# Performance work log

Measured on AMD Instinct MI355X. Metric: run time of the kernel, lower is better.

The kernel has to match this reference:

```python
import jax, jax.numpy as jnp
import numpy as np

CHANNELS = 512
GROUPS = 32
EPS = 1e-6


def setup_inputs() -> dict:
    key = jax.random.key(0)
    ks = jax.random.split(key, 10)
    C = CHANNELS
    s = 1.0 / np.sqrt(C)
    return {
        "hidden_states": jax.random.normal(ks[0], (4, 64, 64, C), dtype=jnp.float32),
        "gn_scale": jnp.ones((C,), dtype=jnp.float32),
        "gn_bias": jnp.zeros((C,), dtype=jnp.float32),
        "wq": jax.random.normal(ks[1], (C, C), dtype=jnp.float32) * s,
        "bq": jnp.zeros((C,), dtype=jnp.float32),
        "wk": jax.random.normal(ks[2], (C, C), dtype=jnp.float32) * s,
        "bk": jnp.zeros((C,), dtype=jnp.float32),
        "wv": jax.random.normal(ks[3], (C, C), dtype=jnp.float32) * s,
        "bv": jnp.zeros((C,), dtype=jnp.float32),
        "wo": jax.random.normal(ks[4], (C, C), dtype=jnp.float32) * s,
        "bo": jnp.zeros((C,), dtype=jnp.float32),
    }


def reference(hidden_states, gn_scale, gn_bias, wq, bq, wk, bk, wv, bv, wo, bo):
    B, H, W, C = hidden_states.shape
    residual = hidden_states
    L = H * W
    x = hidden_states.reshape(B, L, C)

    # GroupNorm: stats over (spatial, channels-within-group), per batch per group
    xg = x.reshape(B, L, GROUPS, C // GROUPS)
    mean = jnp.mean(xg, axis=(1, 3), keepdims=True)
    var = jnp.var(xg, axis=(1, 3), keepdims=True)
    xn = ((xg - mean) * jax.lax.rsqrt(var + EPS)).reshape(B, L, C)
    xn = xn * gn_scale + gn_bias

    # QKV projections (heads=1, head_dim=C)
    q = xn @ wq + bq
    k = xn @ wk + bk
    v = xn @ wv + bv

    scale = 1.0 / jnp.sqrt(jnp.asarray(C, dtype=q.dtype))
    scores = jnp.einsum('bld,bsd->bls', q, k) * scale  # [B, L, L]
    attn = jax.nn.softmax(scores, axis=-1)
    out = jnp.einsum('bls,bsd->bld', attn, v)

    out = out @ wo + bo
    return out.reshape(B, H, W, C) + residual
```

## Files before the change

kernel.cpp:

```cpp
#include <hip/hip_runtime.h>
#include <hip/hip_bf16.h>
#include <stdint.h>

#define BATCH 4
#define SEQ   4096
#define CH    512
#define NGRP  32
#define GEPS  1e-6f

typedef short  short8  __attribute__((ext_vector_type(8)));
typedef float  floatx4 __attribute__((ext_vector_type(4)));

static __device__ __forceinline__ short bf16b(float f) {
    __hip_bfloat16 h = __float2bfloat16(f);
    return __builtin_bit_cast(short, h);
}
static __device__ __forceinline__ float bf2f(short s) {
    unsigned u = ((unsigned)(unsigned short)s) << 16;
    return __builtin_bit_cast(float, u);
}
static __device__ __forceinline__ char fp8b(float f) {
    int pk = __builtin_amdgcn_cvt_pk_fp8_f32(f, f, 0, false);
    return (char)(pk & 0xff);
}

static __device__ __forceinline__ void dma16(const void* g, void* l) {
    __builtin_amdgcn_global_load_lds(
        (const __attribute__((address_space(1))) unsigned int*)g,
        (__attribute__((address_space(3))) unsigned int*)l, 16, 0, 0);
}

static __device__ __forceinline__ float rowmax16(float x) {
    int xi = __builtin_bit_cast(int, x);
    x = fmaxf(x, __builtin_bit_cast(float, __builtin_amdgcn_update_dpp(xi, xi, 0x128, 0xf, 0xf, true)));
    xi = __builtin_bit_cast(int, x);
    x = fmaxf(x, __builtin_bit_cast(float, __builtin_amdgcn_update_dpp(xi, xi, 0x124, 0xf, 0xf, true)));
    xi = __builtin_bit_cast(int, x);
    x = fmaxf(x, __builtin_bit_cast(float, __builtin_amdgcn_update_dpp(xi, xi, 0x122, 0xf, 0xf, true)));
    xi = __builtin_bit_cast(int, x);
    x = fmaxf(x, __builtin_bit_cast(float, __builtin_amdgcn_update_dpp(xi, xi, 0x121, 0xf, 0xf, true)));
    return x;
}

__global__ __launch_bounds__(256) void gn_partial_kernel(const float* __restrict__ x,
                                                         float* __restrict__ statsraw) {
    int blk = blockIdx.x;
    int t = threadIdx.x;
    size_t row0 = (size_t)blk * 64;
    int qd = t & 127;
    int rh = t >> 7;
    const float* base = x + row0 * 512 + qd * 4;
    float s1 = 0.f, s2 = 0.f;
    #pragma unroll 4
    for (int i = 0; i < 32; ++i) {
        int r = rh + i * 2;
        float4 v = *reinterpret_cast<const float4*>(base + (size_t)r * 512);
        s1 += v.x + v.y + v.z + v.w;
        s2 += v.x * v.x + v.y * v.y + v.z * v.z + v.w * v.w;
    }
    __shared__ float a1[256], a2[256];
    a1[t] = s1; a2[t] = s2;
    __syncthreads();
    if (t < 32) {
        float u1 = 0.f, u2 = 0.f;
        #pragma unroll
        for (int e = 0; e < 4; ++e) {
            u1 += a1[t * 4 + e] + a1[128 + t * 4 + e];
            u2 += a2[t * 4 + e] + a2[128 + t * 4 + e];
        }
        int b = (int)(row0 >> 12);
        atomicAdd(&statsraw[(b * 32 + t) * 2],     u1);
        atomicAdd(&statsraw[(b * 32 + t) * 2 + 1], u2);
    }
}

__global__ __launch_bounds__(256) void gn_apply_kernel(const float* __restrict__ x,
                                                       const float* __restrict__ statsraw,
                                                       const float* __restrict__ gsc,
                                                       const float* __restrict__ gbs,
                                                       short* __restrict__ xn) {
    int i4 = blockIdx.x * 256 + threadIdx.x;
    int base = i4 * 4;
    int b = base >> 21;
    int c = base & 511;
    int sidx = (b * 32 + (c >> 4)) * 2;
    float s1 = statsraw[sidx], s2 = statsraw[sidx + 1];
    float mean = s1 * (1.f / 65536.f);
    float var  = s2 * (1.f / 65536.f) - mean * mean;
    float rstd = rsqrtf(var + GEPS);
    float4 xv = reinterpret_cast<const float4*>(x)[i4];
    float4 sv = *reinterpret_cast<const float4*>(gsc + c);
    float4 bv = *reinterpret_cast<const float4*>(gbs + c);
    union { short s[4]; uint2 u; } p;
    p.s[0] = bf16b((xv.x - mean) * rstd * sv.x + bv.x);
    p.s[1] = bf16b((xv.y - mean) * rstd * sv.y + bv.y);
    p.s[2] = bf16b((xv.z - mean) * rstd * sv.z + bv.z);
    p.s[3] = bf16b((xv.w - mean) * rstd * sv.w + bv.w);
    reinterpret_cast<uint2*>(xn)[i4] = p.u;
}

__global__ __launch_bounds__(256) void wtrans_kernel(const float* __restrict__ w0,
                                                     const float* __restrict__ w1,
                                                     const float* __restrict__ w2,
                                                     const float* __restrict__ w3,
                                                     short* __restrict__ wT) {
    const float* w = (blockIdx.z == 0) ? w0 : (blockIdx.z == 1) ? w1
                   : (blockIdx.z == 2) ? w2 : w3;
    short* out = wT + (size_t)blockIdx.z * CH * CH;
    int n0 = blockIdx.x * 32, k0 = blockIdx.y * 32;
    int tx = threadIdx.x, ty = threadIdx.y;
    __shared__ float s[32][33];
    #pragma unroll
    for (int i = 0; i < 4; ++i) {
        int kk = ty + i * 8;
        s[kk][tx] = w[(size_t)(k0 + kk) * CH + n0 + tx];
    }
    __syncthreads();
    #pragma unroll
    for (int i = 0; i < 4; ++i) {
        int nn = ty + i * 8;
        out[(size_t)(n0 + nn) * CH + k0 + tx] = bf16b(s[tx][nn]);
    }
}

__global__ __launch_bounds__(256) void gemm_qkv_kernel(const short* __restrict__ A,
                                                       const short* __restrict__ wT,
                                                       const float* __restrict__ bq,
                                                       const float* __restrict__ bk,
                                                       const float* __restrict__ bv,
                                                       char* __restrict__ q8,
                                                       char* __restrict__ k8,
                                                       char* __restrict__ vT8) {
    __shared__ short As[128 * 64];
    __shared__ short Bs[128 * 64];
    __shared__ char  vls[128 * 144];
    int m0 = blockIdx.x * 128;
    int nblk = blockIdx.y;
    int which = nblk >> 2;
    int n0 = (nblk & 3) * 128;
    const short* BT = wT + (size_t)which * 512 * 512;
    const float* bias = (which == 0) ? bq : (which == 1) ? bk : bv;
    int t = threadIdx.x;
    int w = t >> 6, lane = t & 63;
    int wr = w >> 1, wc = w & 1;
    int l15 = lane & 15, l4 = lane >> 4;
    floatx4 acc[4][4];
    #pragma unroll
    for (int i = 0; i < 4; ++i)
        #pragma unroll
        for (int j = 0; j < 4; ++j) acc[i][j] = (floatx4){0.f, 0.f, 0.f, 0.f};

    for (int k0 = 0; k0 < 512; k0 += 64) {
        __syncthreads();
        #pragma unroll
        for (int i = 0; i < 4; ++i) {
            int c = i * 256 + t;
            int row = c >> 3, j = (c & 7) ^ (row & 7);
            dma16(&A[(size_t)(m0 + row) * 512 + k0 + j * 8], &As[(c & ~63) * 8]);
            dma16(&BT[(size_t)(n0 + row) * 512 + k0 + j * 8], &Bs[(c & ~63) * 8]);
        }
        __syncthreads();
        #pragma unroll
        for (int kk = 0; kk < 64; kk += 32) {
            short8 af[4], bf[4];
            #pragma unroll
            for (int i = 0; i < 4; ++i) {
                int row = wr * 64 + i * 16 + l15;
                int j = (kk >> 3) + l4;
                af[i] = *reinterpret_cast<const short8*>(&As[(row * 8 + (j ^ (l15 & 7))) * 8]);
            }
            #pragma unroll
            for (int j2 = 0; j2 < 4; ++j2) {
                int row = wc * 64 + j2 * 16 + l15;
                int j = (kk >> 3) + l4;
                bf[j2] = *reinterpret_cast<const short8*>(&Bs[(row * 8 + (j ^ (l15 & 7))) * 8]);
            }
            #pragma unroll
            for (int i = 0; i < 4; ++i)
                #pragma unroll
                for (int j2 = 0; j2 < 4; ++j2)
                    acc[i][j2] = __builtin_amdgcn_mfma_f32_16x16x32_bf16(af[i], bf[j2], acc[i][j2], 0, 0, 0);
        }
    }
    if (which < 2) {
        char* o8 = (which == 0) ? q8 : k8;
        #pragma unroll
        for (int i = 0; i < 4; ++i)
            #pragma unroll
            for (int j = 0; j < 4; ++j)
                #pragma unroll
                for (int r = 0; r < 4; ++r) {
                    int row = m0 + wr * 64 + i * 16 + l4 * 4 + r;
                    int col = n0 + wc * 64 + j * 16 + l15;
                    o8[(size_t)row * 512 + col] = fp8b(acc[i][j][r] + bias[col]);
                }
    } else {
        __syncthreads();
        #pragma unroll
        for (int i = 0; i < 4; ++i)
            #pragma unroll
            for (int j = 0; j < 4; ++j)
                #pragma unroll
                for (int r = 0; r < 4; ++r) {
                    int rl = wr * 64 + i * 16 + l4 * 4 + r;
                    int cl = wc * 64 + j * 16 + l15;
                    vls[cl * 144 + rl] = fp8b(acc[i][j][r] + bias[n0 + cl]);
                }
        __syncthreads();
        int b = m0 >> 12, l0 = m0 & 4095;
        #pragma unroll
        for (int p = 0; p < 4; ++p) {
            int slot = p * 256 + t;
            int c = slot >> 3, off = (slot & 7) * 16;
            uint4 v = *reinterpret_cast<const uint4*>(&vls[c * 144 + off]);
            *reinterpret_cast<uint4*>(&vT8[((size_t)b * 512 + n0 + c) * 4096 + l0 + off]) = v;
        }
    }
}

__global__ __launch_bounds__(256) void gemm_bt_kernel(const short* __restrict__ A,
                                                      const short* __restrict__ BT,
                                                      const float* __restrict__ bias,
                                                      float* __restrict__ outf,
                                                      const float* __restrict__ resid) {
    __shared__ short As[128 * 64];
    __shared__ short Bs[128 * 64];
    int m0 = blockIdx.x * 128, n0 = blockIdx.y * 128;
    int t = threadIdx.x;
    int w = t >> 6, lane = t & 63;
    int wr = w >> 1, wc = w & 1;
    int l15 = lane & 15, l4 = lane >> 4;
    floatx4 acc[4][4];
    #pragma unroll
    for (int i = 0; i < 4; ++i)
        #pragma unroll
        for (int j = 0; j < 4; ++j) acc[i][j] = (floatx4){0.f, 0.f, 0.f, 0.f};

    for (int k0 = 0; k0 < 512; k0 += 64) {
        __syncthreads();
        #pragma unroll
        for (int i = 0; i < 4; ++i) {
            int c = i * 256 + t;
            int row = c >> 3, j = (c & 7) ^ (row & 7);
            dma16(&A[(size_t)(m0 + row) * 512 + k0 + j * 8], &As[(c & ~63) * 8]);
            dma16(&BT[(size_t)(n0 + row) * 512 + k0 + j * 8], &Bs[(c & ~63) * 8]);
        }
        __syncthreads();
        #pragma unroll
        for (int kk = 0; kk < 64; kk += 32) {
            short8 af[4], bf[4];
            #pragma unroll
            for (int i = 0; i < 4; ++i) {
                int row = wr * 64 + i * 16 + l15;
                int j = (kk >> 3) + l4;
                af[i] = *reinterpret_cast<const short8*>(&As[(row * 8 + (j ^ (l15 & 7))) * 8]);
            }
            #pragma unroll
            for (int j2 = 0; j2 < 4; ++j2) {
                int row = wc * 64 + j2 * 16 + l15;
                int j = (kk >> 3) + l4;
                bf[j2] = *reinterpret_cast<const short8*>(&Bs[(row * 8 + (j ^ (l15 & 7))) * 8]);
            }
            #pragma unroll
            for (int i = 0; i < 4; ++i)
                #pragma unroll
                for (int j2 = 0; j2 < 4; ++j2)
                    acc[i][j2] = __builtin_amdgcn_mfma_f32_16x16x32_bf16(af[i], bf[j2], acc[i][j2], 0, 0, 0);
        }
    }
    #pragma unroll
    for (int i = 0; i < 4; ++i)
        #pragma unroll
        for (int j = 0; j < 4; ++j)
            #pragma unroll
            for (int r = 0; r < 4; ++r) {
                int row = m0 + wr * 64 + i * 16 + l4 * 4 + r;
                int col = n0 + wc * 64 + j * 16 + l15;
                float vv = acc[i][j][r] + bias[col];
                outf[(size_t)row * 512 + col] = vv + resid[(size_t)row * 512 + col];
            }
}

__global__ __launch_bounds__(256, 2) void flash_kernel(const char* __restrict__ q8,
                                                       const char* __restrict__ k8,
                                                       const char* __restrict__ v8,
                                                       short* __restrict__ Opart,
                                                       float* __restrict__ ml) {
    __shared__ __align__(16) char smem[68096];
    int bx = blockIdx.x;
    int pb = bx & 7;
    int part = pb >> 2, b = pb & 3;
    int q0 = (bx >> 3) * 64;
    int t = threadIdx.x, w = t >> 6, lane = t & 63;
    int l15 = lane & 15, l4 = lane >> 4;
    const float scale = 0.044194173824159216f;

    long qf[16];
    {
        const char* qrow = q8 + ((size_t)b * SEQ + q0 + w * 16 + l15) * 512;
        #pragma unroll
        for (int ks = 0; ks < 16; ++ks)
            qf[ks] = *reinterpret_cast<const long*>(qrow + ks * 32 + l4 * 8);
    }

    floatx4 acc[32];
    #pragma unroll
    for (int i = 0; i < 32; ++i) acc[i] = (floatx4){0.f, 0.f, 0.f, 0.f};
    floatx4 lacc = (floatx4){0.f, 0.f, 0.f, 0.f};
    float mused[4] = {-1e30f, -1e30f, -1e30f, -1e30f};

    const long ones = 0x3838383838383838L;

    const char* kbase = k8 + (size_t)b * SEQ * 512;
    const char* vbase = v8 + (size_t)b * 512 * SEQ;

    const int kswz = l15 & 7;
    const int vswz = (l4 >> 1) ^ ((l15 >> 2) & 1);
    const int koff = (l4 & 1) * 8;
    const int s_begin = part * (SEQ / 2);

    auto stage = [&](int s0, int buf) {
        char* Kd = smem + buf * 16384;
        char* Vd = smem + 32768 + buf * 16384;
        #pragma unroll
        for (int i = 0; i < 4; ++i) {
            int c = i * 256 + t;
            int row = c >> 5, j = (c & 31) ^ (row & 7);
            dma16(kbase + (size_t)(s0 + row) * 512 + j * 16, Kd + (size_t)(c & ~63) * 16);
        }
        #pragma unroll
        for (int i = 0; i < 4; ++i) {
            int c = i * 256 + t;
            int d = c >> 1, j = (c & 1) ^ ((d >> 2) & 1);
            dma16(vbase + (size_t)d * SEQ + s0 + j * 16, Vd + (size_t)(c & ~63) * 16);
        }
    };

    stage(s_begin, 0);
    __syncthreads();

    for (int it = 0; it < 64; ++it) {
        int cur = it & 1;
        if (it + 1 < 64) stage(s_begin + (it + 1) * 32, 1 - cur);

        const char* Kb = smem + cur * 16384;
        const char* Vb = smem + 32768 + cur * 16384;

        floatx4 sa0 = (floatx4){0.f, 0.f, 0.f, 0.f};
        floatx4 sa1 = (floatx4){0.f, 0.f, 0.f, 0.f};
        #pragma unroll
        for (int ks = 0; ks < 16; ++ks) {
            int jc = ks * 2 + (l4 >> 1);
            int a0 = (l15 * 32 + (jc ^ kswz)) * 16 + koff;
            long b0 = *reinterpret_cast<const long*>(Kb + a0);
            long b1 = *reinterpret_cast<const long*>(Kb + a0 + 8192);
            sa0 = __builtin_amdgcn_mfma_f32_16x16x32_fp8_fp8(qf[ks], b0, sa0, 0, 0, 0);
            sa1 = __builtin_amdgcn_mfma_f32_16x16x32_fp8_fp8(qf[ks], b1, sa1, 0, 0, 0);
        }

        float v0[4], v1[4], nm4[4];
        bool need = false;
        #pragma unroll
        for (int r = 0; r < 4; ++r) {
            v0[r] = sa0[r] * scale; v1[r] = sa1[r] * scale;
            nm4[r] = rowmax16(fmaxf(v0[r], v1[r]));
            need |= (nm4[r] > mused[r] + 5.0f);
        }
        if (__ballot(need)) {
            #pragma unroll
            for (int r = 0; r < 4; ++r) {
                float nm = fmaxf(mused[r], nm4[r]);
                float al = __expf(mused[r] - nm);
                lacc[r] *= al;
                #pragma unroll
                for (int i = 0; i < 32; ++i) acc[i][r] *= al;
                mused[r] = nm;
            }
        }
        float p0[4], p1[4];
        #pragma unroll
        for (int r = 0; r < 4; ++r) {
            p0[r] = __expf(v0[r] - mused[r]);
            p1[r] = __expf(v1[r] - mused[r]);
        }

        char* Ps = smem + 65536 + w * 640;
        #pragma unroll
        for (int r = 0; r < 4; ++r) {
            int pk = __builtin_amdgcn_cvt_pk_fp8_f32(p0[r], p1[r], 0, false);
            Ps[(l4 * 4 + r) * 40 + l15]      = (char)(pk & 0xff);
            Ps[(l4 * 4 + r) * 40 + 16 + l15] = (char)((pk >> 8) & 0xff);
        }

        long pf = *reinterpret_cast<const long*>(Ps + l15 * 40 + l4 * 8);
        lacc = __builtin_amdgcn_mfma_f32_16x16x32_fp8_fp8(pf, ones, lacc, 0, 0, 0);
        #pragma unroll
        for (int tt = 0; tt < 32; ++tt) {
            int d = tt * 16 + l15;
            long vf = *reinterpret_cast<const long*>(Vb + (d * 2 + vswz) * 16 + koff);
            acc[tt] = __builtin_amdgcn_mfma_f32_16x16x32_fp8_fp8(pf, vf, acc[tt], 0, 0, 0);
        }

        __syncthreads();
    }

    short* obase = Opart + (((size_t)part * BATCH + b) * SEQ + q0 + w * 16) * 512;
    #pragma unroll
    for (int r = 0; r < 4; ++r) {
        #pragma unroll
        for (int tt = 0; tt < 32; ++tt)
            obase[(size_t)(l4 * 4 + r) * 512 + tt * 16 + l15] = bf16b(acc[tt][r]);
    }
    if (l15 == 0) {
        #pragma unroll
        for (int r = 0; r < 4; ++r) {
            size_t rowg = ((size_t)part * BATCH + b) * SEQ + q0 + w * 16 + l4 * 4 + r;
            ml[rowg * 2]     = mused[r];
            ml[rowg * 2 + 1] = lacc[r];
        }
    }
}

__global__ __launch_bounds__(256) void combine_kernel(const short* __restrict__ Opart,
                                                      const float* __restrict__ ml,
                                                      short* __restrict__ attn) {
    int i8 = blockIdx.x * 256 + threadIdx.x;
    size_t row = (size_t)i8 >> 6;
    float m0 = ml[row * 2], l0 = ml[row * 2 + 1];
    float m1 = ml[((size_t)BATCH * SEQ + row) * 2], l1 = ml[((size_t)BATCH * SEQ + row) * 2 + 1];
    float m = fmaxf(m0, m1);
    float e0 = __expf(m0 - m), e1 = __expf(m1 - m);
    float inv = 1.f / (e0 * l0 + e1 * l1);
    e0 *= inv; e1 *= inv;
    union { uint4 u; short s[8]; } a, bb, o;
    a.u  = reinterpret_cast<const uint4*>(Opart)[i8];
    bb.u = reinterpret_cast<const uint4*>(Opart)[(size_t)BATCH * SEQ * 512 / 8 + i8];
    #pragma unroll
    for (int e = 0; e < 8; ++e)
        o.s[e] = bf16b(bf2f(a.s[e]) * e0 + bf2f(bb.s[e]) * e1);
    reinterpret_cast<uint4*>(attn)[i8] = o.u;
}

extern "C" void kernel_launch(void* const* d_in, const int* in_sizes, int n_in,
                              void* d_out, int out_size, void* d_ws, size_t ws_size,
                              hipStream_t stream) {
    const float* x   = (const float*)d_in[0];
    const float* gsc = (const float*)d_in[1];
    const float* gbs = (const float*)d_in[2];
    const float* wq  = (const float*)d_in[3];
    const float* bq  = (const float*)d_in[4];
    const float* wk  = (const float*)d_in[5];
    const float* bk  = (const float*)d_in[6];
    const float* wv  = (const float*)d_in[7];
    const float* bv  = (const float*)d_in[8];
    const float* wo  = (const float*)d_in[9];
    const float* bo  = (const float*)d_in[10];
    float* out = (float*)d_out;

    char* ws = (char*)d_ws;
    const size_t MB = 1ull << 20;
    short* xn    = (short*)ws;
    char*  q8    = (char*)(ws + 16 * MB);
    char*  k8    = (char*)(ws + 24 * MB);
    char*  vT8   = (char*)(ws + 32 * MB);
    short* Opart = (short*)(ws + 40 * MB);
    short* wT    = (short*)(ws + 72 * MB);
    float* stats = (float*)(ws + 74 * MB);
    float* ml    = (float*)(ws + 74 * MB + 65536);
    short* attn  = xn;

    hipMemsetAsync(stats, 0, 256 * sizeof(float), stream);
    gn_partial_kernel<<<256, 256, 0, stream>>>(x, stats);
    gn_apply_kernel<<<8192, 256, 0, stream>>>(x, stats, gsc, gbs, xn);
    wtrans_kernel<<<dim3(16, 16, 4), dim3(32, 8), 0, stream>>>(wq, wk, wv, wo, wT);

    short* woT = wT + 786432;

    gemm_qkv_kernel<<<dim3(128, 12), 256, 0, stream>>>(xn, wT, bq, bk, bv, q8, k8, vT8);
    flash_kernel<<<512, 256, 0, stream>>>(q8, k8, vT8, Opart, ml);
    combine_kernel<<<4096, 256, 0, stream>>>(Opart, ml, attn);
    gemm_bt_kernel<<<dim3(128, 4), 256, 0, stream>>>(attn, woT, bo, out, x);
}
```

Measured before the change: 331.8 us.

## Fuse split-softmax combine into output projection GEMM A-tile load

Removes the separate combine kernel and merges the two flash-attention partial outputs inside the output-projection GEMM while staging the A tile into shared memory. This drops one kernel launch and the write-then-reread of the combined attention tensor. In exchange, each of the four column-block GEMM workgroups recomputes the merge and reads both partials, and the A tile now goes through registers instead of the async DMA path. The change also permutes the row order in the V-transpose shared buffer of the QKV GEMM and packs the fp8 P stores in the flash kernel into 16-bit writes.

After: 320.8 us. 1.03x faster.

```diff
diff --git a/kernel.cpp b/kernel.cpp
--- a/kernel.cpp
+++ b/kernel.cpp
@@ -203,8 +203,9 @@
                 #pragma unroll
                 for (int r = 0; r < 4; ++r) {
                     int rl = wr * 64 + i * 16 + l4 * 4 + r;
+                    int rp = (rl & ~31) | (((rl & 15) << 1) | ((rl >> 4) & 1));
                     int cl = wc * 64 + j * 16 + l15;
-                    vls[cl * 144 + rl] = fp8b(acc[i][j][r] + bias[n0 + cl]);
+                    vls[cl * 144 + rp] = fp8b(acc[i][j][r] + bias[n0 + cl]);
                 }
         __syncthreads();
         int b = m0 >> 12, l0 = m0 & 4095;
@@ -212,13 +213,15 @@
         for (int p = 0; p < 4; ++p) {
             int slot = p * 256 + t;
             int c = slot >> 3, off = (slot & 7) * 16;
-            uint4 v = *reinterpret_cast<const uint4*>(&vls[c * 144 + off]);
+            uint4 v;
+            __builtin_memcpy(&v, &vls[c * 144 + off], 16);
             *reinterpret_cast<uint4*>(&vT8[((size_t)b * 512 + n0 + c) * 4096 + l0 + off]) = v;
         }
     }
 }
 
-__global__ __launch_bounds__(256) void gemm_bt_kernel(const short* __restrict__ A,
+__global__ __launch_bounds__(256) void gemm_bt_kernel(const short* __restrict__ Opart,
+                                                      const float* __restrict__ ml,
                                                       const short* __restrict__ BT,
                                                       const float* __restrict__ bias,
                                                       float* __restrict__ outf,
@@ -230,6 +233,7 @@
     int w = t >> 6, lane = t & 63;
     int wr = w >> 1, wc = w & 1;
     int l15 = lane & 15, l4 = lane >> 4;
+    const size_t PART = (size_t)BATCH * SEQ;
     floatx4 acc[4][4];
     #pragma unroll
     for (int i = 0; i < 4; ++i)
@@ -241,9 +245,25 @@
         #pragma unroll
         for (int i = 0; i < 4; ++i) {
             int c = i * 256 + t;
-            int row = c >> 3, j = (c & 7) ^ (row & 7);
-            dma16(&A[(size_t)(m0 + row) * 512 + k0 + j * 8], &As[(c & ~63) * 8]);
-            dma16(&BT[(size_t)(n0 + row) * 512 + k0 + j * 8], &Bs[(c & ~63) * 8]);
+            int rl = c >> 3, j = (c & 7) ^ (rl & 7);
+            size_t rowg = (size_t)(m0 + rl);
+            const short* s0 = Opart + rowg * 512 + k0 + j * 8;
+            const short* s1 = s0 + PART * 512;
+            uint4 a0 = *reinterpret_cast<const uint4*>(s0);
+            uint4 a1 = *reinterpret_cast<const uint4*>(s1);
+            float mA = ml[rowg * 2],          lA = ml[rowg * 2 + 1];
+            float mB = ml[(PART + rowg) * 2], lB = ml[(PART + rowg) * 2 + 1];
+            float mm = fmaxf(mA, mB);
+            float e0 = __expf(mA - mm), e1 = __expf(mB - mm);
+            float inv = 1.f / (e0 * lA + e1 * lB);
+            e0 *= inv; e1 *= inv;
+            union { uint4 u; short s[8]; } ua, ub, uo;
+            ua.u = a0; ub.u = a1;
+            #pragma unroll
+            for (int e = 0; e < 8; ++e)
+                uo.s[e] = bf16b(bf2f(ua.s[e]) * e0 + bf2f(ub.s[e]) * e1);
+            *reinterpret_cast<uint4*>(&As[c * 8]) = uo.u;
+            dma16(&BT[(size_t)(n0 + rl) * 512 + k0 + j * 8], &Bs[(c & ~63) * 8]);
         }
         __syncthreads();
         #pragma unroll
@@ -388,11 +408,11 @@
         #pragma unroll
         for (int r = 0; r < 4; ++r) {
             int pk = __builtin_amdgcn_cvt_pk_fp8_f32(p0[r], p1[r], 0, false);
-            Ps[(l4 * 4 + r) * 40 + l15]      = (char)(pk & 0xff);
-            Ps[(l4 * 4 + r) * 40 + 16 + l15] = (char)((pk >> 8) & 0xff);
-        }
-
-        long pf = *reinterpret_cast<const long*>(Ps + l15 * 40 + l4 * 8);
+            *reinterpret_cast<short*>(Ps + (l4 * 4 + r) * 40 + l15 * 2) = (short)pk;
+        }
+
+        long pf;
+        __builtin_memcpy(&pf, (const char*)__builtin_assume_aligned(Ps + l15 * 40 + l4 * 8, 8), 8);
         lacc = __builtin_amdgcn_mfma_f32_16x16x32_fp8_fp8(pf, ones, lacc, 0, 0, 0);
         #pragma unroll
         for (int tt = 0; tt < 32; ++tt) {
@@ -419,26 +439,6 @@
             ml[rowg * 2 + 1] = lacc[r];
         }
     }
-}
-
-__global__ __launch_bounds__(256) void combine_kernel(const short* __restrict__ Opart,
-                                                      const float* __restrict__ ml,
-                                                      short* __restrict__ attn) {
-    int i8 = blockIdx.x * 256 + threadIdx.x;
-    size_t row = (size_t)i8 >> 6;
-    float m0 = ml[row * 2], l0 = ml[row * 2 + 1];
-    float m1 = ml[((size_t)BATCH * SEQ + row) * 2], l1 = ml[((size_t)BATCH * SEQ + row) * 2 + 1];
-    float m = fmaxf(m0, m1);
-    float e0 = __expf(m0 - m), e1 = __expf(m1 - m);
-    float inv = 1.f / (e0 * l0 + e1 * l1);
-    e0 *= inv; e1 *= inv;
-    union { uint4 u; short s[8]; } a, bb, o;
-    a.u  = reinterpret_cast<const uint4*>(Opart)[i8];
-    bb.u = reinterpret_cast<const uint4*>(Opart)[(size_t)BATCH * SEQ * 512 / 8 + i8];
-    #pragma unroll
-    for (int e = 0; e < 8; ++e)
-        o.s[e] = bf16b(bf2f(a.s[e]) * e0 + bf2f(bb.s[e]) * e1);
-    reinterpret_cast<uint4*>(attn)[i8] = o.u;
 }
 
 extern "C" void kernel_launch(void* const* d_in, const int* in_sizes, int n_in,
@@ -467,7 +467,6 @@
     short* wT    = (short*)(ws + 72 * MB);
     float* stats = (float*)(ws + 74 * MB);
     float* ml    = (float*)(ws + 74 * MB + 65536);
-    short* attn  = xn;
 
     hipMemsetAsync(stats, 0, 256 * sizeof(float), stream);
     gn_partial_kernel<<<256, 256, 0, stream>>>(x, stats);
@@ -478,6 +477,5 @@
 
     gemm_qkv_kernel<<<dim3(128, 12), 256, 0, stream>>>(xn, wT, bq, bk, bv, q8, k8, vT8);
     flash_kernel<<<512, 256, 0, stream>>>(q8, k8, vT8, Opart, ml);
-    combine_kernel<<<4096, 256, 0, stream>>>(Opart, ml, attn);
-    gemm_bt_kernel<<<dim3(128, 4), 256, 0, stream>>>(attn, woT, bo, out, x);
-}
+    gemm_bt_kernel<<<dim3(128, 4), 256, 0, stream>>>(Opart, ml, woT, bo, out, x);
+}
```
